# Optimization experiments

Measured on AMD Instinct MI355X. Metric: run time of the kernel, lower is better.

Reference implementation:

```python
import jax, jax.numpy as jnp
import numpy as np

B, SEQ, D = 4, 1024, 1024
H = 16
HD = D // H            # 64, matches cos/sin last dim
S_COLS, TOPK = 8, 2
INTER = 768            # find_multiple(round(1.0 * D * 2 / 3), 256)
EPS = 1e-5


def setup_inputs() -> dict:
    key = jax.random.key(0)
    ks = jax.random.split(key, 6)
    hidden_states = jax.random.normal(ks[0], (B, SEQ, D), jnp.float32)
    # RoPE tables (standard rotary, theta=10000)
    inv_freq = 1.0 / (10000.0 ** (jnp.arange(0, HD, 2, dtype=jnp.float32) / HD))
    freqs = jnp.outer(jnp.arange(SEQ, dtype=jnp.float32), inv_freq)
    emb = jnp.concatenate([freqs, freqs], axis=-1)  # [SEQ, HD]
    cos, sin = jnp.cos(emb), jnp.sin(emb)
    Wr = jax.random.normal(ks[1], (S_COLS, D), jnp.float32) * 0.02
    temperature = jnp.ones((1,), jnp.float32)
    # Stacked per-column TransformerBlock params (bias-free linears)
    Wqkv = jax.random.normal(ks[2], (S_COLS, D, 3 * D), jnp.float32) * 0.02
    Wo = jax.random.normal(ks[3], (S_COLS, D, D), jnp.float32) * 0.02
    Wgu = jax.random.normal(ks[4], (S_COLS, D, 2 * INTER), jnp.float32) * 0.02
    Wd = jax.random.normal(ks[5], (S_COLS, INTER, D), jnp.float32) * 0.02
    return dict(hidden_states=hidden_states, cos=cos, sin=sin, Wr=Wr,
                temperature=temperature, Wqkv=Wqkv, Wo=Wo, Wgu=Wgu, Wd=Wd)


def _rms_norm(x):
    return x * jax.lax.rsqrt(jnp.mean(x * x, axis=-1, keepdims=True) + EPS)


def _rotate_half(x):
    x1, x2 = jnp.split(x, 2, axis=-1)
    return jnp.concatenate([-x2, x1], axis=-1)


def _columns_forward(x, Wqkv, Wo, Wgu, Wd, cos, sin):
    # x: [n, seq, D] dispatched sequences; params gathered per dispatch entry [n, ...]
    n, seq, d = x.shape
    qkv = jnp.einsum('nsd,nde->nse', x, Wqkv)
    q, k, v = jnp.split(qkv, 3, axis=-1)
    q = q.reshape(n, seq, H, HD)
    k = k.reshape(n, seq, H, HD)
    v = v.reshape(n, seq, H, HD)
    c = cos[None, :, None, :]
    s = sin[None, :, None, :]
    q = q * c + _rotate_half(q) * s
    k = k * c + _rotate_half(k) * s
    scores = jnp.einsum('nqhd,nkhd->nhqk', q, k) / jnp.sqrt(jnp.asarray(HD, x.dtype))
    attn = jax.nn.softmax(scores, axis=-1)  # non-causal (HRM-style block)
    ctx = jnp.einsum('nhqk,nkhd->nqhd', attn, v).reshape(n, seq, d)
    attn_out = jnp.einsum('nsd,nde->nse', ctx, Wo)
    x = _rms_norm(x + attn_out)                      # post-norm residual
    gu = jnp.einsum('nsd,nde->nse', x, Wgu)
    gate, up = jnp.split(gu, 2, axis=-1)
    mlp_out = jnp.einsum('nsi,nid->nsd', jax.nn.silu(gate) * up, Wd)
    return _rms_norm(x + mlp_out)


def reference(hidden_states, cos, sin, Wr, temperature, Wqkv, Wo, Wgu, Wd):
    Bn = hidden_states.shape[0]
    temp = jnp.clip(temperature, 0.1, 10.0)
    routing_logits = (hidden_states.mean(axis=1) @ Wr.T) / temp   # [B, S]
    topk_vals, topk_idx = jax.lax.top_k(routing_logits, TOPK)
    weights = jax.nn.softmax(topk_vals, axis=-1)                  # [B, k]
    flat_idx = topk_idx.reshape(-1)                               # [B*k] expert ids
    flat_w = weights.reshape(-1)
    sample_idx = jnp.repeat(jnp.arange(Bn), TOPK)                 # [B*k]
    # Sparse dispatch: exactly B*k block forwards via per-entry param gather
    x_disp = hidden_states[sample_idx]
    col_out = _columns_forward(x_disp, Wqkv[flat_idx], Wo[flat_idx],
                               Wgu[flat_idx], Wd[flat_idx], cos, sin)
    result = jnp.zeros_like(hidden_states).at[sample_idx].add(
        flat_w[:, None, None] * col_out)
    return result, routing_logits
```

## Files before the change

### kernel.cpp

```cpp
#include <hip/hip_runtime.h>
#include <hip/hip_bf16.h>
#include <math.h>

#define B_     4
#define SEQ_   1024
#define D_     1024
#define H_     16
#define NE_    8
#define INTER_ 768
#define EPS_   1e-5f

typedef unsigned short u16;
typedef __attribute__((ext_vector_type(8))) short s8v;
typedef __attribute__((ext_vector_type(4))) short s4v;
typedef __attribute__((ext_vector_type(4))) float f4v;
typedef __attribute__((ext_vector_type(4))) unsigned short u16x4;
typedef __attribute__((ext_vector_type(8))) unsigned short u16x8;

__device__ __forceinline__ u16 f2bf(float x) {
    union { float f; unsigned u; } c; c.f = x;
    unsigned r = (c.u + 0x7FFFu + ((c.u >> 16) & 1u)) >> 16;
    return (u16)r;
}
__device__ __forceinline__ float bf2f(u16 h) {
    union { unsigned u; float f; } c; c.u = ((unsigned)h) << 16;
    return c.f;
}
__device__ __forceinline__ unsigned pk2(float a, float b) {
    union { float f; unsigned u; } x, y; x.f = a; y.f = b;
    return ((x.u + 0x8000u) >> 16) | ((y.u + 0x8000u) & 0xffff0000u);
}

#define GLDS16(gp, lp) \
    __builtin_amdgcn_global_load_lds((const __attribute__((address_space(1))) unsigned int*)(gp), \
                                     (__attribute__((address_space(3))) unsigned int*)(lp), 16, 0, 0)

__global__ void route1(const float* __restrict__ hidden, float* __restrict__ part,
                       u16* __restrict__ hb) {
    int b = blockIdx.x, ch = blockIdx.y, t = threadIdx.x;
    const float* xb = hidden + (size_t)b * SEQ_ * D_ + (size_t)ch * 32 * D_;
    u16* ho = hb + (size_t)b * SEQ_ * D_ + (size_t)ch * 32 * D_;
    float4 acc = make_float4(0.f, 0.f, 0.f, 0.f);
    for (int r = 0; r < 32; ++r) {
        float4 v = *(const float4*)&xb[(size_t)r * D_ + t * 4];
        acc.x += v.x; acc.y += v.y; acc.z += v.z; acc.w += v.w;
        u16x4 o = {f2bf(v.x), f2bf(v.y), f2bf(v.z), f2bf(v.w)};
        *(u16x4*)&ho[(size_t)r * D_ + t * 4] = o;
    }
    *(float4*)&part[((size_t)(b * 32 + ch)) * D_ + t * 4] = acc;
}

__global__ void route2(const float* __restrict__ part, const float* __restrict__ Wr,
                       const float* __restrict__ temp, float* __restrict__ out_logits,
                       int* __restrict__ flat_idx, float* __restrict__ flat_w) {
    __shared__ float col[1024];
    __shared__ float sm[8];
    int b = blockIdx.x, t = threadIdx.x;
    float4 s = make_float4(0.f, 0.f, 0.f, 0.f);
    for (int ch = 0; ch < 32; ++ch) {
        float4 v = *(const float4*)&part[((size_t)(b * 32 + ch)) * D_ + t * 4];
        s.x += v.x; s.y += v.y; s.z += v.z; s.w += v.w;
    }
    col[t * 4 + 0] = s.x * (1.f / 1024.f);
    col[t * 4 + 1] = s.y * (1.f / 1024.f);
    col[t * 4 + 2] = s.z * (1.f / 1024.f);
    col[t * 4 + 3] = s.w * (1.f / 1024.f);
    __syncthreads();
    int j = t >> 5, d0 = t & 31;
    float p = 0.f;
    for (int d = d0; d < 1024; d += 32) p += col[d] * Wr[j * 1024 + d];
    for (int off = 16; off >= 1; off >>= 1) p += __shfl_down(p, off, 32);
    if (d0 == 0) sm[j] = p;
    __syncthreads();
    if (t == 0) {
        float tc = temp[0];
        tc = fminf(fmaxf(tc, 0.1f), 10.0f);
        float lg[8];
        for (int jj = 0; jj < 8; ++jj) {
            lg[jj] = sm[jj] / tc;
            out_logits[b * 8 + jj] = lg[jj];
        }
        int i0 = 0; float v0 = lg[0];
        for (int jj = 1; jj < 8; ++jj) if (lg[jj] > v0) { v0 = lg[jj]; i0 = jj; }
        int i1 = -1; float v1 = -1e30f;
        for (int jj = 0; jj < 8; ++jj) if (jj != i0 && lg[jj] > v1) { v1 = lg[jj]; i1 = jj; }
        float e1 = expf(v1 - v0);
        flat_idx[2 * b]     = i0;
        flat_idx[2 * b + 1] = i1;
        flat_w[2 * b]       = 1.0f / (1.0f + e1);
        flat_w[2 * b + 1]   = e1 / (1.0f + e1);
    }
}

__global__ __launch_bounds__(256) void wtrans_all(const float* __restrict__ Wqkv,
                                                  const float* __restrict__ Wo,
                                                  const float* __restrict__ Wgu,
                                                  const float* __restrict__ Wd,
                                                  u16* __restrict__ WqkvT, u16* __restrict__ WoT,
                                                  u16* __restrict__ WguT, u16* __restrict__ WdT) {
    int bid = blockIdx.x;
    const float* W; u16* Wt; int K, N, nx, gu = 0;
    if (bid < 6144)      { W = Wqkv; Wt = WqkvT; K = 1024; N = 3072; nx = 48; }
    else if (bid < 8192) { bid -= 6144;  W = Wo;  Wt = WoT;  K = 1024; N = 1024; nx = 16; }
    else if (bid < 11264){ bid -= 8192;  W = Wgu; Wt = WguT; K = 1024; N = 1536; nx = 24; gu = 1; }
    else                 { bid -= 11264; W = Wd;  Wt = WdT;  K = 768;  N = 1024; nx = 16; }
    int x = bid % nx; bid /= nx;
    int ny = K >> 6;
    int y = bid % ny;
    int e = bid / ny;

    __shared__ float tile[64][65];
    int k0 = y * 64, n0 = x * 64;
    const float* Wp = W + (size_t)e * K * N;
    u16* Wtp = Wt + (size_t)e * K * N;
    int t = threadIdx.x;
    int kk = t >> 4, ns = t & 15;
#pragma unroll
    for (int p = 0; p < 4; ++p) {
        float4 v = *(const float4*)&Wp[(size_t)(k0 + kk + p * 16) * N + n0 + ns * 4];
        tile[kk + p * 16][ns * 4 + 0] = v.x;
        tile[kk + p * 16][ns * 4 + 1] = v.y;
        tile[kk + p * 16][ns * 4 + 2] = v.z;
        tile[kk + p * 16][ns * 4 + 3] = v.w;
    }
    __syncthreads();
    int nn = t >> 3, ks = t & 7;
#pragma unroll
    for (int p = 0; p < 2; ++p) {
        int n = n0 + nn + p * 32;
        int nd = n;
        if (gu) nd = (n < 768) ? ((n >> 4) << 5) + (n & 15)
                               : (((n - 768) >> 4) << 5) + 16 + (n & 15);
        u16x8 o;
#pragma unroll
        for (int jj = 0; jj < 8; ++jj) o[jj] = f2bf(tile[ks * 8 + jj][nn + p * 32]);
        *(u16x8*)&Wtp[(size_t)nd * K + k0 + ks * 8] = o;
    }
}

#define GEMM_CORE(A, Wt, K)                                                                 \
    f4v acc[4][4];                                                                          \
    _Pragma("unroll") for (int i = 0; i < 4; ++i)                                           \
        _Pragma("unroll") for (int jj = 0; jj < 4; ++jj) acc[i][jj] = (f4v){0.f,0.f,0.f,0.f}; \
    for (int k0 = 0; k0 < K; k0 += 32) {                                                    \
        _Pragma("unroll") for (int it = 0; it < 2; ++it) {                                  \
            int p = it * 256 + w * 64 + lane;                                               \
            int row = p >> 2, seg = (p & 3) ^ ((row >> 1) & 3);                             \
            GLDS16(A  + (size_t)(m0 + row) * K + k0 + seg * 8, As + (size_t)(it*256 + w*64) * 8); \
            GLDS16(Wt + (size_t)(n0 + row) * K + k0 + seg * 8, Bs + (size_t)(it*256 + w*64) * 8); \
        }                                                                                   \
        __syncthreads();                                                                    \
        s8v af[4], bfr[4];                                                                  \
        _Pragma("unroll") for (int ti = 0; ti < 4; ++ti) {                                  \
            int r = wm + ti * 16 + c;                                                       \
            af[ti]  = *(const s8v*)&As[r * 32 + (g ^ ((r >> 1) & 3)) * 8];                   \
        }                                                                                   \
        _Pragma("unroll") for (int tj = 0; tj < 4; ++tj) {                                  \
            int r = wn + tj * 16 + c;                                                       \
            bfr[tj] = *(const s8v*)&Bs[r * 32 + (g ^ ((r >> 1) & 3)) * 8];                   \
        }                                                                                   \
        _Pragma("unroll") for (int ti = 0; ti < 4; ++ti)                                    \
            _Pragma("unroll") for (int tj = 0; tj < 4; ++tj)                                \
                acc[ti][tj] = __builtin_amdgcn_mfma_f32_16x16x32_bf16(af[ti], bfr[tj], acc[ti][tj], 0, 0, 0); \
        __syncthreads();                                                                    \
    }

__global__ __launch_bounds__(256) void gemm_bf16(const u16* __restrict__ Abase,
                                                 const u16* __restrict__ Wtbase,
                                                 u16* __restrict__ Cb,
                                                 const int* __restrict__ flat_idx,
                                                 int M, int N, int K, int aDiv) {
    __shared__ __align__(16) u16 As[128 * 32];
    __shared__ __align__(16) u16 Bs[128 * 32];
    int e = blockIdx.z;
    const u16* A  = Abase + (size_t)(e / aDiv) * M * K;
    const u16* Wt = Wtbase + (size_t)flat_idx[e] * N * K;
    int m0 = blockIdx.y * 128, n0 = blockIdx.x * 128;
    int t = threadIdx.x, lane = t & 63, w = t >> 6;
    int g = lane >> 4, c = lane & 15;
    int wm = (w >> 1) * 64, wn = (w & 1) * 64;

    GEMM_CORE(A, Wt, K)

    u16* C = Cb + (size_t)e * M * N;
#pragma unroll
    for (int ti = 0; ti < 4; ++ti)
#pragma unroll
        for (int tj = 0; tj < 4; ++tj)
#pragma unroll
            for (int i = 0; i < 4; ++i)
                C[(size_t)(m0 + wm + ti * 16 + g * 4 + i) * N + n0 + wn + tj * 16 + c] = f2bf(acc[ti][tj][i]);
}

__global__ __launch_bounds__(256) void gemm_qkv(const u16* __restrict__ Abase,
                                                const u16* __restrict__ Wtbase,
                                                const int* __restrict__ flat_idx,
                                                const float* __restrict__ cosb,
                                                const float* __restrict__ sinb,
                                                u16* __restrict__ Qb, u16* __restrict__ Kb,
                                                u16* __restrict__ Vb) {
    __shared__ __align__(16) u16 As[128 * 32];
    __shared__ __align__(16) u16 Bs[128 * 32];
    const int K = 1024, N = 3072;
    int e = blockIdx.z;
    const u16* A  = Abase + (size_t)(e >> 1) * 1024 * K;
    const u16* Wt = Wtbase + (size_t)flat_idx[e] * N * K;
    int m0 = blockIdx.y * 128, n0 = blockIdx.x * 128;
    int t = threadIdx.x, lane = t & 63, w = t >> 6;
    int g = lane >> 4, c = lane & 15;
    int wm = (w >> 1) * 64, wn = (w & 1) * 64;

    GEMM_CORE(A, Wt, K)

    int col0 = n0 + wn;
    int sb = m0 + wm + g * 4;
    if (col0 < 2048) {
        bool isq = col0 < 1024;
        u16* dst = isq ? Qb : Kb;
        int h = (col0 & 1023) >> 6;
        const float scl = isq ? 0.125f * 1.44269504f : 1.0f;
#pragma unroll
        for (int ti = 0; ti < 4; ++ti)
#pragma unroll
            for (int i = 0; i < 4; ++i) {
                int s = sb + ti * 16 + i;
                size_t ob = ((size_t)(e * 1024) + s) * 1024 + h * 64;
#pragma unroll
                for (int tj = 0; tj < 2; ++tj) {
                    int d = tj * 16 + c;
                    float x1 = acc[ti][tj][i], x2 = acc[ti][tj + 2][i];
                    float c1 = cosb[s * 64 + d],      s1 = sinb[s * 64 + d];
                    float c2 = cosb[s * 64 + d + 32], s2 = sinb[s * 64 + d + 32];
                    dst[ob + d]      = f2bf((x1 * c1 - x2 * s1) * scl);
                    dst[ob + d + 32] = f2bf((x2 * c2 + x1 * s2) * scl);
                }
            }
    } else {
        int vcol = col0 - 2048;
#pragma unroll
        for (int ti = 0; ti < 4; ++ti)
#pragma unroll
            for (int tj = 0; tj < 4; ++tj)
#pragma unroll
                for (int i = 0; i < 4; ++i)
                    Vb[((size_t)(e * 1024) + sb + ti * 16 + i) * 1024 + vcol + tj * 16 + c] = f2bf(acc[ti][tj][i]);
    }
}

__global__ __launch_bounds__(256) void gemm_wgu_silu(const u16* __restrict__ Abase,
                                                     const u16* __restrict__ Wtbase,
                                                     u16* __restrict__ act,
                                                     const int* __restrict__ flat_idx) {
    __shared__ __align__(16) u16 As[128 * 32];
    __shared__ __align__(16) u16 Bs[128 * 32];
    const int K = 1024, N = 1536;
    int e = blockIdx.z;
    const u16* A  = Abase + (size_t)e * 1024 * K;
    const u16* Wt = Wtbase + (size_t)flat_idx[e] * N * K;
    int m0 = blockIdx.y * 128, n0 = blockIdx.x * 128;
    int t = threadIdx.x, lane = t & 63, w = t >> 6;
    int g = lane >> 4, c = lane & 15;
    int wm = (w >> 1) * 64, wn = (w & 1) * 64;

    GEMM_CORE(A, Wt, K)

    int col0 = n0 + wn;
    int oc0 = (col0 >> 1) + c;
    int sb = m0 + wm + g * 4;
#pragma unroll
    for (int ti = 0; ti < 4; ++ti)
#pragma unroll
        for (int i = 0; i < 4; ++i) {
            size_t rb = ((size_t)(e * 1024) + sb + ti * 16 + i) * 768;
#pragma unroll
            for (int pr = 0; pr < 2; ++pr) {
                float gt = acc[ti][pr * 2][i];
                float up = acc[ti][pr * 2 + 1][i];
                act[rb + oc0 + pr * 16] = f2bf(gt / (1.f + __expf(-gt)) * up);
            }
        }
}

__global__ __launch_bounds__(256) void vtrans(const u16* __restrict__ Vb, u16* __restrict__ Vtg) {
    __shared__ __align__(16) u16 tile[64 * 72];
    int s0 = blockIdx.x * 64;
    int eh = blockIdx.y;
    int e = eh >> 4, h = eh & 15;
    int t = threadIdx.x;
#pragma unroll
    for (int it = 0; it < 2; ++it) {
        int p = it * 256 + t;
        int sr = p >> 3, ds = p & 7;
        u16x8 v = *(const u16x8*)&Vb[((size_t)(e * 1024) + s0 + sr) * 1024 + h * 64 + ds * 8];
        *(u16x8*)&tile[sr * 72 + ds * 8] = v;
    }
    __syncthreads();
#pragma unroll
    for (int it = 0; it < 2; ++it) {
        int p = it * 256 + t;
        int d = p >> 3, ks = p & 7;
        u16x8 o;
#pragma unroll
        for (int jj = 0; jj < 8; ++jj) o[jj] = tile[(ks * 8 + jj) * 72 + d];
        *(u16x8*)&Vtg[((size_t)((e * 16 + h) * 64) + d) * 1024 + s0 + ks * 8] = o;
    }
}

__global__ __launch_bounds__(256) void attn_mfma(const u16* __restrict__ Qb, const u16* __restrict__ Kb,
                                                 const u16* __restrict__ Vtg, u16* __restrict__ ctx) {
    __shared__ __align__(16) u16 Ks[64 * 64];
    __shared__ __align__(16) u16 Vt[64 * 64];
    int e = blockIdx.x, h = blockIdx.y, qt = blockIdx.z;
    int t = threadIdx.x, lane = t & 63, w = t >> 6;
    int g = lane >> 4, c = lane & 15;
    int q0 = qt * 64 + w * 16;

    s8v qf[2];
#pragma unroll
    for (int ks = 0; ks < 2; ++ks)
        qf[ks] = *(const s8v*)&Qb[((size_t)(e * 1024) + q0 + c) * 1024 + h * 64 + ks * 32 + g * 8];

    f4v O[4];
#pragma unroll
    for (int tj = 0; tj < 4; ++tj) O[tj] = (f4v){0.f, 0.f, 0.f, 0.f};
    f4v liacc = (f4v){0.f, 0.f, 0.f, 0.f};
    const s4v vone = {(short)0x3F80, (short)0x3F80, (short)0x3F80, (short)0x3F80};

    for (int kt = 0; kt < 16; ++kt) {
#pragma unroll
        for (int it = 0; it < 2; ++it) {
            int p = it * 256 + w * 64 + lane;
            int row = p >> 3, ss = p & 7;
            GLDS16(Kb + ((size_t)(e * 1024 + kt * 64 + row)) * 1024 + h * 64 + (ss ^ (row & 7)) * 8,
                   Ks + (size_t)(it * 256 + w * 64) * 8);
            GLDS16(Vtg + ((size_t)((e * 16 + h) * 64 + row)) * 1024 + kt * 64 + (ss ^ (row & 7)) * 8,
                   Vt + (size_t)(it * 256 + w * 64) * 8);
        }
        __syncthreads();

        f4v st[4];
#pragma unroll
        for (int tj = 0; tj < 4; ++tj) st[tj] = (f4v){0.f, 0.f, 0.f, 0.f};
#pragma unroll
        for (int ks = 0; ks < 2; ++ks)
#pragma unroll
            for (int tj = 0; tj < 4; ++tj) {
                int kvl = tj * 16 + c;
                s8v kf = *(const s8v*)&Ks[kvl * 64 + (((ks * 4 + g) ^ (kvl & 7)) * 8)];
                st[tj] = __builtin_amdgcn_mfma_f32_16x16x32_bf16(kf, qf[ks], st[tj], 0, 0, 0);
            }

        s4v pf[4];
#pragma unroll
        for (int tj = 0; tj < 4; ++tj) {
            float p0 = __builtin_amdgcn_exp2f(st[tj][0]);
            float p1 = __builtin_amdgcn_exp2f(st[tj][1]);
            float p2 = __builtin_amdgcn_exp2f(st[tj][2]);
            float p3 = __builtin_amdgcn_exp2f(st[tj][3]);
            union { unsigned u[2]; s4v v; } pu;
            pu.u[0] = pk2(p0, p1);
            pu.u[1] = pk2(p2, p3);
            pf[tj] = pu.v;
        }

#pragma unroll
        for (int tjC = 0; tjC < 4; ++tjC) {
            liacc = __builtin_amdgcn_mfma_f32_16x16x16bf16_1k(pf[tjC], vone, liacc, 0, 0, 0);
#pragma unroll
            for (int tjd = 0; tjd < 4; ++tjd) {
                int d = tjd * 16 + c;
                int sd = tjC * 2 + (g >> 1);
                s4v vf = *(const s4v*)&Vt[d * 64 + ((sd ^ (d & 7)) * 8) + (g & 1) * 4];
                O[tjd] = __builtin_amdgcn_mfma_f32_16x16x16bf16_1k(pf[tjC], vf, O[tjd], 0, 0, 0);
            }
        }
        __syncthreads();
    }
#pragma unroll
    for (int i = 0; i < 4; ++i) {
        float linv = 1.0f / liacc[i];
        size_t rbase = ((size_t)(e * 1024) + q0 + g * 4 + i) * 1024 + h * 64;
#pragma unroll
        for (int tjd = 0; tjd < 4; ++tjd)
            ctx[rbase + tjd * 16 + c] = f2bf(O[tjd][i] * linv);
    }
}

__global__ void add_rmsnorm(const u16* __restrict__ hb, const u16* __restrict__ aob,
                            u16* __restrict__ xnb) {
    int row = blockIdx.x;
    int e = row >> 10;
    int b = e >> 1;
    int s = row & 1023;
    const u16* xr = hb + (((size_t)b * SEQ_ + s) << 10);
    const u16* ar = aob + ((size_t)row << 10);
    u16* o = xnb + ((size_t)row << 10);
    int t = threadIdx.x;
    u16x4 xv = *(const u16x4*)&xr[t * 4];
    u16x4 av = *(const u16x4*)&ar[t * 4];
    float v[4];
    float ss = 0.f;
#pragma unroll
    for (int i = 0; i < 4; ++i) {
        v[i] = bf2f(xv[i]) + bf2f(av[i]);
        ss += v[i] * v[i];
    }
    for (int off = 32; off >= 1; off >>= 1) ss += __shfl_down(ss, off, 64);
    __shared__ float wred[4];
    if ((t & 63) == 0) wred[t >> 6] = ss;
    __syncthreads();
    float tot = wred[0] + wred[1] + wred[2] + wred[3];
    float scale = rsqrtf(tot * (1.0f / 1024.0f) + EPS_);
    u16x4 ov;
#pragma unroll
    for (int i = 0; i < 4; ++i) ov[i] = f2bf(v[i] * scale);
    *(u16x4*)&o[t * 4] = ov;
}

__global__ void final_kernel(const u16* __restrict__ xnb, const u16* __restrict__ mlpb,
                             const float* __restrict__ flat_w, float* __restrict__ out) {
    int row = blockIdx.x;
    int b = row >> 10;
    int s = row & 1023;
    int t = threadIdx.x;
    __shared__ float wred[4];
    float res[4] = {0.f, 0.f, 0.f, 0.f};
    for (int j = 0; j < 2; ++j) {
        int e = 2 * b + j;
        size_t off = (((size_t)e * SEQ_ + s) << 10);
        u16x4 xv = *(const u16x4*)&xnb[off + t * 4];
        u16x4 mv = *(const u16x4*)&mlpb[off + t * 4];
        float v[4];
        float ss = 0.f;
#pragma unroll
        for (int i = 0; i < 4; ++i) {
            v[i] = bf2f(xv[i]) + bf2f(mv[i]);
            ss += v[i] * v[i];
        }
        for (int off2 = 32; off2 >= 1; off2 >>= 1) ss += __shfl_down(ss, off2, 64);
        if ((t & 63) == 0) wred[t >> 6] = ss;
        __syncthreads();
        float tot = wred[0] + wred[1] + wred[2] + wred[3];
        float scale = rsqrtf(tot * (1.0f / 1024.0f) + EPS_);
        float wgt = flat_w[e];
#pragma unroll
        for (int i = 0; i < 4; ++i) res[i] += wgt * v[i] * scale;
        __syncthreads();
    }
    float* o = out + ((size_t)row << 10);
    *(float4*)&o[t * 4] = make_float4(res[0], res[1], res[2], res[3]);
}

extern "C" void kernel_launch(void* const* d_in, const int* in_sizes, int n_in,
                              void* d_out, int out_size, void* d_ws, size_t ws_size,
                              hipStream_t stream) {
    const float* hidden = (const float*)d_in[0];
    const float* cosb   = (const float*)d_in[1];
    const float* sinb   = (const float*)d_in[2];
    const float* Wr     = (const float*)d_in[3];
    const float* temp   = (const float*)d_in[4];
    const float* Wqkv   = (const float*)d_in[5];
    const float* Wo     = (const float*)d_in[6];
    const float* Wgu    = (const float*)d_in[7];
    const float* Wd     = (const float*)d_in[8];
    float* out = (float*)d_out;
    float* out_logits = out + (size_t)B_ * SEQ_ * D_;

    char* base = (char*)d_ws;
    int*   flat_idx = (int*)base;
    float* flat_w   = (float*)(base + 128);
    float* routeP   = (float*)(base + 4096);
    size_t off = (size_t)1 << 20;
    u16* WqkvT = (u16*)(base + off); off += (size_t)8 * 3072 * 1024 * 2;
    u16* WoT   = (u16*)(base + off); off += (size_t)8 * 1024 * 1024 * 2;
    u16* WguT  = (u16*)(base + off); off += (size_t)8 * 1536 * 1024 * 2;
    u16* WdT   = (u16*)(base + off); off += (size_t)8 * 1024 * 768 * 2;
    u16* hb    = (u16*)(base + off); off += (size_t)4 * 1024 * 1024 * 2;
    u16* Qb    = (u16*)(base + off); off += (size_t)8 * 1024 * 1024 * 2;
    u16* Kb    = (u16*)(base + off); off += (size_t)8 * 1024 * 1024 * 2;
    u16* Vb    = (u16*)(base + off); off += (size_t)8 * 1024 * 1024 * 2;
    u16* Vtg   = (u16*)(base + off); off += (size_t)8 * 1024 * 1024 * 2;
    u16* ctxb  = (u16*)(base + off); off += (size_t)8 * 1024 * 1024 * 2;
    u16* aob   = (u16*)(base + off); off += (size_t)8 * 1024 * 1024 * 2;
    u16* xnb   = (u16*)(base + off); off += (size_t)8 * 1024 * 1024 * 2;
    u16* actb  = (u16*)(base + off); off += (size_t)8 * 1024 * 768 * 2;
    u16* mlpb  = (u16*)(base + off); off += (size_t)8 * 1024 * 1024 * 2;

    route1<<<dim3(4, 32), 256, 0, stream>>>(hidden, routeP, hb);
    route2<<<4, 256, 0, stream>>>(routeP, Wr, temp, out_logits, flat_idx, flat_w);
    wtrans_all<<<12800, 256, 0, stream>>>(Wqkv, Wo, Wgu, Wd, WqkvT, WoT, WguT, WdT);

    gemm_qkv<<<dim3(24, 8, 8), 256, 0, stream>>>(hb, WqkvT, flat_idx, cosb, sinb, Qb, Kb, Vb);
    vtrans<<<dim3(16, 128), 256, 0, stream>>>(Vb, Vtg);
    attn_mfma<<<dim3(8, 16, 16), 256, 0, stream>>>(Qb, Kb, Vtg, ctxb);
    gemm_bf16<<<dim3(8, 8, 8), 256, 0, stream>>>(ctxb, WoT, aob, flat_idx, 1024, 1024, 1024, 1);
    add_rmsnorm<<<NE_ * SEQ_, 256, 0, stream>>>(hb, aob, xnb);
    gemm_wgu_silu<<<dim3(12, 8, 8), 256, 0, stream>>>(xnb, WguT, actb, flat_idx);
    gemm_bf16<<<dim3(8, 8, 8), 256, 0, stream>>>(actb, WdT, mlpb, flat_idx, 1024, 1024, 768, 1);
    final_kernel<<<B_ * SEQ_, 256, 0, stream>>>(xnb, mlpb, flat_w, out);
}
```

Baseline: 545.3 us.

## Multi-stage LDS pipelining in GEMMs and attention, skip unused expert weight conversion

The shared GEMM core moves to a 3-stage LDS ring filled by asynchronous global-to-LDS loads, with explicit vmcnt waits and raw s_barrier, and raises wave priority around the MFMA block. Attention K/V tiles are double-buffered the same way. The weight transpose/convert kernel now returns early for experts not selected by routing, so it converts only the used experts' weights instead of all eight. The pipelining triples GEMM LDS use, which may lower occupancy, and the hand-written waitcnt counts must match the number of outstanding loads to stay correct.

```diff
diff --git a/kernel.cpp b/kernel.cpp
--- a/kernel.cpp
+++ b/kernel.cpp
@@ -34,6 +34,8 @@
 #define GLDS16(gp, lp) \
     __builtin_amdgcn_global_load_lds((const __attribute__((address_space(1))) unsigned int*)(gp), \
                                      (__attribute__((address_space(3))) unsigned int*)(lp), 16, 0, 0)
+
+#define BARRIER()  asm volatile("s_barrier" ::: "memory")
 
 __global__ void route1(const float* __restrict__ hidden, float* __restrict__ part,
                        u16* __restrict__ hb) {
@@ -97,7 +99,8 @@
                                                   const float* __restrict__ Wgu,
                                                   const float* __restrict__ Wd,
                                                   u16* __restrict__ WqkvT, u16* __restrict__ WoT,
-                                                  u16* __restrict__ WguT, u16* __restrict__ WdT) {
+                                                  u16* __restrict__ WguT, u16* __restrict__ WdT,
+                                                  const int* __restrict__ flat_idx) {
     int bid = blockIdx.x;
     const float* W; u16* Wt; int K, N, nx, gu = 0;
     if (bid < 6144)      { W = Wqkv; Wt = WqkvT; K = 1024; N = 3072; nx = 48; }
@@ -109,6 +112,11 @@
     int y = bid % ny;
     int e = bid / ny;
 
+    bool used = false;
+#pragma unroll
+    for (int jj = 0; jj < 8; ++jj) used |= (flat_idx[jj] == e);
+    if (!used) return;
+
     __shared__ float tile[64][65];
     int k0 = y * 64, n0 = x * 64;
     const float* Wp = W + (size_t)e * K * N;
@@ -138,31 +146,56 @@
     }
 }
 
-#define GEMM_CORE(A, Wt, K)                                                                 \
+#define GEMM_STAGE(Ap_, Wp_, Kp_, k0v, bo)                                                  \
+    {                                                                                       \
+        _Pragma("unroll") for (int it = 0; it < 2; ++it) {                                  \
+            int p = it * 256 + w * 64 + lane;                                               \
+            int row = p >> 2, seg = (p & 3) ^ ((row >> 1) & 3);                             \
+            GLDS16((Ap_) + (size_t)(m0 + row) * (Kp_) + (k0v) + seg * 8,                    \
+                   As + (bo) + (size_t)(it * 256 + w * 64) * 8);                            \
+            GLDS16((Wp_) + (size_t)(n0 + row) * (Kp_) + (k0v) + seg * 8,                    \
+                   Bs + (bo) + (size_t)(it * 256 + w * 64) * 8);                            \
+        }                                                                                   \
+    }
+
+#define GEMM_CORE(Ap_, Wp_, Kp_)                                                            \
     f4v acc[4][4];                                                                          \
     _Pragma("unroll") for (int i = 0; i < 4; ++i)                                           \
         _Pragma("unroll") for (int jj = 0; jj < 4; ++jj) acc[i][jj] = (f4v){0.f,0.f,0.f,0.f}; \
-    for (int k0 = 0; k0 < K; k0 += 32) {                                                    \
-        _Pragma("unroll") for (int it = 0; it < 2; ++it) {                                  \
-            int p = it * 256 + w * 64 + lane;                                               \
-            int row = p >> 2, seg = (p & 3) ^ ((row >> 1) & 3);                             \
-            GLDS16(A  + (size_t)(m0 + row) * K + k0 + seg * 8, As + (size_t)(it*256 + w*64) * 8); \
-            GLDS16(Wt + (size_t)(n0 + row) * K + k0 + seg * 8, Bs + (size_t)(it*256 + w*64) * 8); \
-        }                                                                                   \
-        __syncthreads();                                                                    \
+    const int NT = (Kp_) / 32;                                                              \
+    GEMM_STAGE(Ap_, Wp_, Kp_, 0, 0)                                                         \
+    GEMM_STAGE(Ap_, Wp_, Kp_, 32, 4096)                                                     \
+    GEMM_STAGE(Ap_, Wp_, Kp_, 64, 8192)                                                     \
+    asm volatile("s_waitcnt vmcnt(8)" ::: "memory");                                        \
+    BARRIER();                                                                              \
+    int cb = 0;                                                                             \
+    for (int kt = 0; kt < NT; ++kt) {                                                       \
+        int bo = cb * 4096;                                                                 \
         s8v af[4], bfr[4];                                                                  \
         _Pragma("unroll") for (int ti = 0; ti < 4; ++ti) {                                  \
             int r = wm + ti * 16 + c;                                                       \
-            af[ti]  = *(const s8v*)&As[r * 32 + (g ^ ((r >> 1) & 3)) * 8];                   \
+            af[ti]  = *(const s8v*)&As[bo + r * 32 + (g ^ ((r >> 1) & 3)) * 8];             \
         }                                                                                   \
         _Pragma("unroll") for (int tj = 0; tj < 4; ++tj) {                                  \
             int r = wn + tj * 16 + c;                                                       \
-            bfr[tj] = *(const s8v*)&Bs[r * 32 + (g ^ ((r >> 1) & 3)) * 8];                   \
+            bfr[tj] = *(const s8v*)&Bs[bo + r * 32 + (g ^ ((r >> 1) & 3)) * 8];             \
         }                                                                                   \
+        __builtin_amdgcn_s_setprio(1);                                                      \
         _Pragma("unroll") for (int ti = 0; ti < 4; ++ti)                                    \
             _Pragma("unroll") for (int tj = 0; tj < 4; ++tj)                                \
                 acc[ti][tj] = __builtin_amdgcn_mfma_f32_16x16x32_bf16(af[ti], bfr[tj], acc[ti][tj], 0, 0, 0); \
-        __syncthreads();                                                                    \
+        __builtin_amdgcn_s_setprio(0);                                                      \
+        BARRIER();                                                                          \
+        if (kt + 3 < NT) {                                                                  \
+            GEMM_STAGE(Ap_, Wp_, Kp_, (kt + 3) * 32, bo)                                    \
+            asm volatile("s_waitcnt vmcnt(8)" ::: "memory");                                \
+        } else if (kt + 2 < NT) {                                                           \
+            asm volatile("s_waitcnt vmcnt(4)" ::: "memory");                                \
+        } else {                                                                            \
+            asm volatile("s_waitcnt vmcnt(0)" ::: "memory");                                \
+        }                                                                                   \
+        BARRIER();                                                                          \
+        cb = (cb == 2) ? 0 : cb + 1;                                                        \
     }
 
 __global__ __launch_bounds__(256) void gemm_bf16(const u16* __restrict__ Abase,
@@ -170,8 +203,8 @@
                                                  u16* __restrict__ Cb,
                                                  const int* __restrict__ flat_idx,
                                                  int M, int N, int K, int aDiv) {
-    __shared__ __align__(16) u16 As[128 * 32];
-    __shared__ __align__(16) u16 Bs[128 * 32];
+    __shared__ __align__(16) u16 As[3 * 128 * 32];
+    __shared__ __align__(16) u16 Bs[3 * 128 * 32];
     int e = blockIdx.z;
     const u16* A  = Abase + (size_t)(e / aDiv) * M * K;
     const u16* Wt = Wtbase + (size_t)flat_idx[e] * N * K;
@@ -199,8 +232,8 @@
                                                 const float* __restrict__ sinb,
                                                 u16* __restrict__ Qb, u16* __restrict__ Kb,
                                                 u16* __restrict__ Vb) {
-    __shared__ __align__(16) u16 As[128 * 32];
-    __shared__ __align__(16) u16 Bs[128 * 32];
+    __shared__ __align__(16) u16 As[3 * 128 * 32];
+    __shared__ __align__(16) u16 Bs[3 * 128 * 32];
     const int K = 1024, N = 3072;
     int e = blockIdx.z;
     const u16* A  = Abase + (size_t)(e >> 1) * 1024 * K;
@@ -251,8 +284,8 @@
                                                      const u16* __restrict__ Wtbase,
                                                      u16* __restrict__ act,
                                                      const int* __restrict__ flat_idx) {
-    __shared__ __align__(16) u16 As[128 * 32];
-    __shared__ __align__(16) u16 Bs[128 * 32];
+    __shared__ __align__(16) u16 As[3 * 128 * 32];
+    __shared__ __align__(16) u16 Bs[3 * 128 * 32];
     const int K = 1024, N = 1536;
     int e = blockIdx.z;
     const u16* A  = Abase + (size_t)e * 1024 * K;
@@ -306,10 +339,22 @@
     }
 }
 
+#define ATTN_STAGE(ktv, bo)                                                                 \
+    {                                                                                       \
+        _Pragma("unroll") for (int it = 0; it < 2; ++it) {                                  \
+            int p = it * 256 + w * 64 + lane;                                               \
+            int row = p >> 3, ss = p & 7;                                                   \
+            GLDS16(Kb + ((size_t)(e * 1024 + (ktv) * 64 + row)) * 1024 + h * 64 + (ss ^ (row & 7)) * 8, \
+                   Ks + (bo) + (size_t)(it * 256 + w * 64) * 8);                            \
+            GLDS16(Vtg + ((size_t)((e * 16 + h) * 64 + row)) * 1024 + (ktv) * 64 + (ss ^ (row & 7)) * 8, \
+                   Vt + (bo) + (size_t)(it * 256 + w * 64) * 8);                            \
+        }                                                                                   \
+    }
+
 __global__ __launch_bounds__(256) void attn_mfma(const u16* __restrict__ Qb, const u16* __restrict__ Kb,
                                                  const u16* __restrict__ Vtg, u16* __restrict__ ctx) {
-    __shared__ __align__(16) u16 Ks[64 * 64];
-    __shared__ __align__(16) u16 Vt[64 * 64];
+    __shared__ __align__(16) u16 Ks[2 * 64 * 64];
+    __shared__ __align__(16) u16 Vt[2 * 64 * 64];
     int e = blockIdx.x, h = blockIdx.y, qt = blockIdx.z;
     int t = threadIdx.x, lane = t & 63, w = t >> 6;
     int g = lane >> 4, c = lane & 15;
@@ -326,18 +371,14 @@
     f4v liacc = (f4v){0.f, 0.f, 0.f, 0.f};
     const s4v vone = {(short)0x3F80, (short)0x3F80, (short)0x3F80, (short)0x3F80};
 
+    ATTN_STAGE(0, 0)
+    ATTN_STAGE(1, 4096)
+    asm volatile("s_waitcnt vmcnt(4)" ::: "memory");
+    BARRIER();
+    int cb = 0;
+
     for (int kt = 0; kt < 16; ++kt) {
-#pragma unroll
-        for (int it = 0; it < 2; ++it) {
-            int p = it * 256 + w * 64 + lane;
-            int row = p >> 3, ss = p & 7;
-            GLDS16(Kb + ((size_t)(e * 1024 + kt * 64 + row)) * 1024 + h * 64 + (ss ^ (row & 7)) * 8,
-                   Ks + (size_t)(it * 256 + w * 64) * 8);
-            GLDS16(Vtg + ((size_t)((e * 16 + h) * 64 + row)) * 1024 + kt * 64 + (ss ^ (row & 7)) * 8,
-                   Vt + (size_t)(it * 256 + w * 64) * 8);
-        }
-        __syncthreads();
-
+        int bo = cb * 4096;
         f4v st[4];
 #pragma unroll
         for (int tj = 0; tj < 4; ++tj) st[tj] = (f4v){0.f, 0.f, 0.f, 0.f};
@@ -346,7 +387,7 @@
 #pragma unroll
             for (int tj = 0; tj < 4; ++tj) {
                 int kvl = tj * 16 + c;
-                s8v kf = *(const s8v*)&Ks[kvl * 64 + (((ks * 4 + g) ^ (kvl & 7)) * 8)];
+                s8v kf = *(const s8v*)&Ks[bo + kvl * 64 + (((ks * 4 + g) ^ (kvl & 7)) * 8)];
                 st[tj] = __builtin_amdgcn_mfma_f32_16x16x32_bf16(kf, qf[ks], st[tj], 0, 0, 0);
             }
 
@@ -370,11 +411,20 @@
             for (int tjd = 0; tjd < 4; ++tjd) {
                 int d = tjd * 16 + c;
                 int sd = tjC * 2 + (g >> 1);
-                s4v vf = *(const s4v*)&Vt[d * 64 + ((sd ^ (d & 7)) * 8) + (g & 1) * 4];
+                s4v vf = *(const s4v*)&Vt[bo + d * 64 + ((sd ^ (d & 7)) * 8) + (g & 1) * 4];
                 O[tjd] = __builtin_amdgcn_mfma_f32_16x16x16bf16_1k(pf[tjC], vf, O[tjd], 0, 0, 0);
             }
         }
-        __syncthreads();
+
+        BARRIER();
+        if (kt + 2 < 16) {
+            ATTN_STAGE(kt + 2, bo)
+            asm volatile("s_waitcnt vmcnt(4)" ::: "memory");
+        } else {
+            asm volatile("s_waitcnt vmcnt(0)" ::: "memory");
+        }
+        BARRIER();
+        cb ^= 1;
     }
 #pragma unroll
     for (int i = 0; i < 4; ++i) {
@@ -488,7 +538,7 @@
 
     route1<<<dim3(4, 32), 256, 0, stream>>>(hidden, routeP, hb);
     route2<<<4, 256, 0, stream>>>(routeP, Wr, temp, out_logits, flat_idx, flat_w);
-    wtrans_all<<<12800, 256, 0, stream>>>(Wqkv, Wo, Wgu, Wd, WqkvT, WoT, WguT, WdT);
+    wtrans_all<<<12800, 256, 0, stream>>>(Wqkv, Wo, Wgu, Wd, WqkvT, WoT, WguT, WdT, flat_idx);
 
     gemm_qkv<<<dim3(24, 8, 8), 256, 0, stream>>>(hb, WqkvT, flat_idx, cosb, sinb, Qb, Kb, Vb);
     vtrans<<<dim3(16, 128), 256, 0, stream>>>(Vb, Vtg);
```

Result: faster. 523.2 us (-4.0%).
